# Kernel optimization log

Measured on AMD Instinct MI355X. Metric: run time of the kernel, lower is better.

## Reference

```python
import jax, jax.numpy as jnp
import numpy as np

B, N, M, D = 64, 512, 1024, 128

def setup_inputs() -> dict:
    key = jax.random.key(0)
    ks = jax.random.split(key, 7)
    s = 1.0 / np.sqrt(D)
    return {
        "h_c": jax.random.normal(ks[0], (B, N, D), dtype=jnp.float32),
        "h_p": jax.random.normal(ks[1], (B, M, D), dtype=jnp.float32),
        "U_w": jax.random.normal(ks[2], (D, D), dtype=jnp.float32) * s,
        "U_b": jax.random.normal(ks[3], (D,), dtype=jnp.float32) * s,
        "V_w": jax.random.normal(ks[4], (D, D), dtype=jnp.float32) * s,
        "V_b": jax.random.normal(ks[5], (D,), dtype=jnp.float32) * s,
        "q": jax.random.normal(ks[6], (D,), dtype=jnp.float32),
    }

def reference(h_c, h_p, U_w, U_b, V_w, V_b, q):
    # ReLU-activated linear projections (torch Linear: x @ W.T + b)
    Uc = jax.nn.relu(jnp.einsum('bnd,ed->bne', h_c, U_w) + U_b)  # (B,N,D)
    Vp = jax.nn.relu(jnp.einsum('bmd,ed->bme', h_p, V_w) + V_b)  # (B,M,D)
    # bilinear attention scores and softmax over protein axis
    attn = jnp.einsum('bnd,bmd->bnm', Uc, Vp)                    # (B,N,M)
    weights = jax.nn.softmax(attn, axis=-1)
    context = jnp.einsum('bnm,bmd->bnd', weights, Vp)            # (B,N,D)
    joint = (Uc + context) * q                                   # (B,N,D)
    return joint.mean(axis=1)                                    # (B,D)
```

## Files before the change

kernel.cpp:

```cpp
#include <hip/hip_runtime.h>
#include <hip/hip_bf16.h>
#include <cstdint>

#define BB 64
#define NN 512
#define MM 1024
#define DD 128

typedef __bf16 bf16x8 __attribute__((ext_vector_type(8)));
typedef float f32x4 __attribute__((ext_vector_type(4)));

static __device__ __forceinline__ unsigned short f2bf(float f) {
    union { float f; unsigned int i; } v; v.f = f;
    unsigned int x = v.i;
    x += 0x7FFFu + ((x >> 16) & 1u);
    return (unsigned short)(x >> 16);
}
static __device__ __forceinline__ unsigned int f2bf2(float a, float b) {
    union { __hip_bfloat162 h; unsigned int u; } c;
    c.h = __float22bfloat162_rn(make_float2(a, b));
    return c.u;
}
static __device__ __forceinline__ void async16(const void* g, void* l) {
    __builtin_amdgcn_global_load_lds(
        (const __attribute__((address_space(1))) void*)g,
        (__attribute__((address_space(3))) void*)l, 16, 0, 0);
}

__global__ __launch_bounds__(256, 4) void proj_v_kernel(
    const float* __restrict__ X,
    const float* __restrict__ Wv,
    const float* __restrict__ bias,
    unsigned short* __restrict__ Y,
    unsigned short* __restrict__ YT)
{
    __shared__ __align__(16) unsigned short Ws[128 * 136];
    unsigned short* Ys = Ws;
    unsigned short* Ts = Ws + 8192;
    const int t = threadIdx.x;
    const int lane = t & 63;
    const int wave = t >> 6;
    const int n16 = lane & 15, q = lane >> 4;
    const long row0 = (long)blockIdx.x * 64;

    float4 xv[8];
    {
        const float* xrow = X + (row0 + wave * 16 + n16) * DD + q * 8;
        #pragma unroll
        for (int kk = 0; kk < 4; ++kk) {
            xv[2 * kk]     = *(const float4*)(xrow + kk * 32);
            xv[2 * kk + 1] = *(const float4*)(xrow + kk * 32 + 4);
        }
    }

    {
        const float4* Wg = (const float4*)Wv;
        #pragma unroll
        for (int i = 0; i < 16; ++i) {
            int idx = i * 256 + t;
            float4 v = Wg[idx];
            int off = idx * 4;
            uint2 u = { f2bf2(v.x, v.y), f2bf2(v.z, v.w) };
            *(uint2*)&Ws[(off >> 7) * 136 + (off & 127)] = u;
        }
    }
    __syncthreads();

    f32x4 acc[8];
    #pragma unroll
    for (int j = 0; j < 8; ++j) acc[j] = {0.f, 0.f, 0.f, 0.f};

    #pragma unroll
    for (int kk = 0; kk < 4; ++kk) {
        float4 x0 = xv[2 * kk], x1 = xv[2 * kk + 1];
        union { bf16x8 v; unsigned int u[4]; } a;
        a.u[0] = f2bf2(x0.x, x0.y); a.u[1] = f2bf2(x0.z, x0.w);
        a.u[2] = f2bf2(x1.x, x1.y); a.u[3] = f2bf2(x1.z, x1.w);
        #pragma unroll
        for (int j = 0; j < 8; ++j) {
            bf16x8 b = *(const bf16x8*)&Ws[(j * 16 + n16) * 136 + q * 8 + kk * 32];
            acc[j] = __builtin_amdgcn_mfma_f32_16x16x32_bf16(a.v, b, acc[j], 0, 0, 0);
        }
    }

    unsigned short yb[8][4];
    #pragma unroll
    for (int j = 0; j < 8; ++j) {
        const float bv = bias[j * 16 + n16];
        float y[4];
        #pragma unroll
        for (int r = 0; r < 4; ++r) {
            float v = acc[j][r] + bv;
            y[r] = v > 0.f ? v : 0.f;
        }
        uint2 u = { f2bf2(y[0], y[1]), f2bf2(y[2], y[3]) };
        *(uint2*)&yb[j][0] = u;
    }
    __syncthreads();

    #pragma unroll
    for (int j = 0; j < 8; ++j) {
        const int e = j * 16 + n16;
        #pragma unroll
        for (int r = 0; r < 4; ++r)
            Ys[(wave * 16 + q * 4 + r) * 128 + e] = yb[j][r];
        *(uint2*)&Ts[e * 72 + wave * 16 + q * 4] = *(uint2*)&yb[j][0];
    }
    __syncthreads();

    {
        uint4* dstY = (uint4*)(Y + row0 * DD);
        const long b = row0 >> 10;
        const long mt = (row0 & 1023) >> 6;
        uint4* dstT = (uint4*)(YT + ((b * 16 + mt) * 128) * 64);
        #pragma unroll
        for (int i = 0; i < 4; ++i) {
            int idx = i * 256 + t;
            dstY[idx] = ((const uint4*)Ys)[idx];
            int e = idx >> 3, m = (idx & 7) * 8;
            dstT[idx] = *(const uint4*)&Ts[e * 72 + m];
        }
    }
}

__global__ __launch_bounds__(256, 2) void attn_kernel(
    const float* __restrict__ hc,
    const float* __restrict__ Wu,
    const float* __restrict__ Ub,
    const unsigned short* __restrict__ Vp,
    const unsigned short* __restrict__ VpT,
    float* __restrict__ part)
{
    __shared__ __align__(16) unsigned short smem[37376];
    unsigned short* Ws  = smem;
    unsigned short* Ucs = smem + 17408;
    unsigned short* Ps  = smem + 32768;

    const int t = threadIdx.x;
    const int lane = t & 63;
    const int wave = t >> 6;
    const int n16 = lane & 15, q = lane >> 4;

    const int id = blockIdx.x;
    const int xcd = id & 7;
    const int slot = id >> 3;
    const int b = xcd * 8 + (slot >> 3);
    const int nt = slot & 7;

    const unsigned short* vpb = Vp + (long)b * MM * DD;
    const unsigned short* vtb = VpT + (long)b * MM * DD;

    {
        const float4* Wg = (const float4*)Wu;
        #pragma unroll
        for (int i = 0; i < 16; ++i) {
            int idx = i * 256 + t;
            float4 v = Wg[idx];
            int off = idx * 4;
            uint2 u = { f2bf2(v.x, v.y), f2bf2(v.z, v.w) };
            *(uint2*)&Ws[(off >> 7) * 136 + (off & 127)] = u;
        }
    }
    __syncthreads();

    f32x4 acc[8];
    #pragma unroll
    for (int j = 0; j < 8; ++j) acc[j] = {0.f, 0.f, 0.f, 0.f};
    {
        const float* xrow = hc + ((long)b * NN + nt * 64 + wave * 16 + n16) * DD + q * 8;
        #pragma unroll
        for (int kk = 0; kk < 4; ++kk) {
            float4 x0 = *(const float4*)(xrow + kk * 32);
            float4 x1 = *(const float4*)(xrow + kk * 32 + 4);
            union { bf16x8 v; unsigned int u[4]; } a;
            a.u[0] = f2bf2(x0.x, x0.y); a.u[1] = f2bf2(x0.z, x0.w);
            a.u[2] = f2bf2(x1.x, x1.y); a.u[3] = f2bf2(x1.z, x1.w);
            #pragma unroll
            for (int j = 0; j < 8; ++j) {
                bf16x8 bb = *(const bf16x8*)&Ws[(j * 16 + n16) * 136 + q * 8 + kk * 32];
                acc[j] = __builtin_amdgcn_mfma_f32_16x16x32_bf16(a.v, bb, acc[j], 0, 0, 0);
            }
        }
    }
    float ucred[8];
    #pragma unroll
    for (int j = 0; j < 8; ++j) {
        const float bv = Ub[j * 16 + n16];
        float s = 0.f;
        #pragma unroll
        for (int r = 0; r < 4; ++r) {
            float v = acc[j][r] + bv;
            v = v > 0.f ? v : 0.f;
            s += v;
            Ucs[(wave * 16 + q * 4 + r) * 136 + j * 16 + n16] = f2bf(v);
        }
        ucred[j] = s;
    }
    __syncthreads();

    bf16x8 Bg[4];
    #pragma unroll
    for (int kk = 0; kk < 4; ++kk)
        Bg[kk] = *(const bf16x8*)&Ucs[(wave * 16 + n16) * 136 + q * 8 + kk * 32];

    {
        #pragma unroll
        for (int i = 0; i < 4; ++i) {
            int L = wave * 256 + i * 64 + lane;
            int r = L >> 4, sc = L & 15, c = sc ^ (r & 7);
            async16(vpb + r * 128 + c * 8, smem + wave * 2048 + i * 512);
        }
        #pragma unroll
        for (int i = 0; i < 4; ++i) {
            int L = wave * 256 + i * 64 + lane;
            int r = L >> 3, sc = L & 7, c = sc ^ (r & 7);
            async16(vtb + r * 64 + c * 8, smem + 8192 + wave * 2048 + i * 512);
        }
    }
    __syncthreads();

    f32x4 O[8];
    #pragma unroll
    for (int j = 0; j < 8; ++j) O[j] = {0.f, 0.f, 0.f, 0.f};
    float lpart = 0.f;
    const float LOG2E = 1.44269504088896f;

    for (int mt = 0; mt < 16; ++mt) {
        const unsigned short* Vs  = smem + ((mt & 1) ? 16384 : 0);
        const unsigned short* VTs = Vs + 8192;
        unsigned short* nVs = smem + ((mt & 1) ? 0 : 16384);

        if (mt < 15) {
            const unsigned short* sv = vpb + (mt + 1) * 8192;
            const unsigned short* st = vtb + (mt + 1) * 8192;
            #pragma unroll
            for (int i = 0; i < 4; ++i) {
                int L = wave * 256 + i * 64 + lane;
                int r = L >> 4, sc = L & 15, c = sc ^ (r & 7);
                async16(sv + r * 128 + c * 8, nVs + wave * 2048 + i * 512);
            }
            #pragma unroll
            for (int i = 0; i < 4; ++i) {
                int L = wave * 256 + i * 64 + lane;
                int r = L >> 3, sc = L & 7, c = sc ^ (r & 7);
                async16(st + r * 64 + c * 8, nVs + 8192 + wave * 2048 + i * 512);
            }
        }

        f32x4 S[4];
        #pragma unroll
        for (int j = 0; j < 4; ++j) S[j] = {0.f, 0.f, 0.f, 0.f};
        #pragma unroll
        for (int kk = 0; kk < 4; ++kk) {
            #pragma unroll
            for (int j = 0; j < 4; ++j) {
                int row = j * 16 + n16;
                int col = ((kk * 4 + q) ^ (n16 & 7)) * 8;
                bf16x8 a = *(const bf16x8*)&Vs[row * 128 + col];
                S[j] = __builtin_amdgcn_mfma_f32_16x16x32_bf16(a, Bg[kk], S[j], 0, 0, 0);
            }
        }

        #pragma unroll
        for (int j = 0; j < 4; ++j) {
            float p0 = __builtin_exp2f(S[j][0] * LOG2E);
            float p1 = __builtin_exp2f(S[j][1] * LOG2E);
            float p2 = __builtin_exp2f(S[j][2] * LOG2E);
            float p3 = __builtin_exp2f(S[j][3] * LOG2E);
            lpart += (p0 + p1) + (p2 + p3);
            uint2 u = { f2bf2(p0, p1), f2bf2(p2, p3) };
            *(uint2*)&Ps[wave * 1152 + n16 * 72 + j * 16 + q * 4] = u;
        }

        #pragma unroll
        for (int kk = 0; kk < 2; ++kk) {
            bf16x8 a = *(const bf16x8*)&Ps[wave * 1152 + n16 * 72 + kk * 32 + q * 8];
            #pragma unroll
            for (int j = 0; j < 8; ++j) {
                int row = j * 16 + n16;
                int col = ((kk * 4 + q) ^ (n16 & 7)) * 8;
                bf16x8 bb = *(const bf16x8*)&VTs[row * 64 + col];
                O[j] = __builtin_amdgcn_mfma_f32_16x16x32_bf16(a, bb, O[j], 0, 0, 0);
            }
        }
        __syncthreads();
    }

    lpart += __shfl_xor(lpart, 16);
    lpart += __shfl_xor(lpart, 32);

    float inv[4];
    #pragma unroll
    for (int r = 0; r < 4; ++r)
        inv[r] = 1.0f / __shfl(lpart, q * 4 + r);

    float* red = (float*)Ps;
    #pragma unroll
    for (int j = 0; j < 8; ++j) {
        float s = ucred[j]
                + O[j][0] * inv[0] + O[j][1] * inv[1]
                + O[j][2] * inv[2] + O[j][3] * inv[3];
        s += __shfl_xor(s, 16);
        s += __shfl_xor(s, 32);
        if (q == 0)
            red[wave * 128 + j * 16 + n16] = s;
    }
    __syncthreads();
    if (t < 128) {
        float tot = red[t] + red[128 + t] + red[256 + t] + red[384 + t];
        part[(long)(b * 8 + nt) * DD + t] = tot;
    }
}

__global__ __launch_bounds__(256) void finalize_kernel(
    const float* __restrict__ part, const float* __restrict__ qv,
    float* __restrict__ out)
{
    int i = blockIdx.x * 256 + threadIdx.x;
    int b = i >> 7, d = i & 127;
    const float* p = part + (long)b * 8 * DD + d;
    float s = 0.f;
    #pragma unroll
    for (int nt = 0; nt < 8; ++nt) s += p[nt * DD];
    out[i] = s * qv[d] * (1.0f / (float)NN);
}

extern "C" void kernel_launch(void* const* d_in, const int* in_sizes, int n_in,
                              void* d_out, int out_size, void* d_ws, size_t ws_size,
                              hipStream_t stream) {
    const float* h_c = (const float*)d_in[0];
    const float* h_p = (const float*)d_in[1];
    const float* U_w = (const float*)d_in[2];
    const float* U_b = (const float*)d_in[3];
    const float* V_w = (const float*)d_in[4];
    const float* V_b = (const float*)d_in[5];
    const float* qv  = (const float*)d_in[6];
    float* out = (float*)d_out;

    unsigned short* Vp  = (unsigned short*)d_ws;
    unsigned short* VpT = Vp + (size_t)BB * MM * DD;
    float* part = (float*)(VpT + (size_t)BB * MM * DD);

    proj_v_kernel<<<BB * MM / 64, 256, 0, stream>>>(h_p, V_w, V_b, Vp, VpT);
    attn_kernel<<<512, 256, 0, stream>>>(h_c, U_w, U_b, Vp, VpT, part);
    finalize_kernel<<<32, 256, 0, stream>>>(part, qv, out);
}
```

Before: 130.8 us.

## Split score tile by key rows across waves and fold log2e into Uc

The QK^T-like score stage is repartitioned so each wave loads only its own 16 Vp rows from LDS and multiplies them against all 64 query rows, whose Uc fragments are held in registers (Bg[4][4]). Previously every wave read all 64 Vp rows. The P tile is now shared through LDS across waves, so a block barrier is needed before the PV stage, and the row sums are reduced across waves through LDS at the end. Folding LOG2E into Uc before the bf16 conversion removes a multiply per exp. The costs are more registers, an extra barrier per tile, and a tiny change in rounding.

New measurement: 129.8 us. Within noise of the previous version (-0.8%).

```diff
diff --git a/kernel.cpp b/kernel.cpp
--- a/kernel.cpp
+++ b/kernel.cpp
@@ -150,6 +150,8 @@
     const unsigned short* vpb = Vp + (long)b * MM * DD;
     const unsigned short* vtb = VpT + (long)b * MM * DD;
 
+    const float LOG2E = 1.44269504088896f;
+
     {
         const float4* Wg = (const float4*)Wu;
         #pragma unroll
@@ -192,16 +194,18 @@
             float v = acc[j][r] + bv;
             v = v > 0.f ? v : 0.f;
             s += v;
-            Ucs[(wave * 16 + q * 4 + r) * 136 + j * 16 + n16] = f2bf(v);
+            Ucs[(wave * 16 + q * 4 + r) * 136 + j * 16 + n16] = f2bf(v * LOG2E);
         }
         ucred[j] = s;
     }
     __syncthreads();
 
-    bf16x8 Bg[4];
-    #pragma unroll
-    for (int kk = 0; kk < 4; ++kk)
-        Bg[kk] = *(const bf16x8*)&Ucs[(wave * 16 + n16) * 136 + q * 8 + kk * 32];
+    bf16x8 Bg[4][4];
+    #pragma unroll
+    for (int j = 0; j < 4; ++j)
+        #pragma unroll
+        for (int kk = 0; kk < 4; ++kk)
+            Bg[j][kk] = *(const bf16x8*)&Ucs[(j * 16 + n16) * 136 + q * 8 + kk * 32];
 
     {
         #pragma unroll
@@ -222,13 +226,37 @@
     f32x4 O[8];
     #pragma unroll
     for (int j = 0; j < 8; ++j) O[j] = {0.f, 0.f, 0.f, 0.f};
-    float lpart = 0.f;
-    const float LOG2E = 1.44269504088896f;
+    float lpart[4] = {0.f, 0.f, 0.f, 0.f};
 
     for (int mt = 0; mt < 16; ++mt) {
         const unsigned short* Vs  = smem + ((mt & 1) ? 16384 : 0);
         const unsigned short* VTs = Vs + 8192;
         unsigned short* nVs = smem + ((mt & 1) ? 0 : 16384);
+
+        f32x4 S[4];
+        #pragma unroll
+        for (int j = 0; j < 4; ++j) S[j] = {0.f, 0.f, 0.f, 0.f};
+        #pragma unroll
+        for (int kk = 0; kk < 4; ++kk) {
+            int row = wave * 16 + n16;
+            int col = ((kk * 4 + q) ^ (n16 & 7)) * 8;
+            bf16x8 a = *(const bf16x8*)&Vs[row * 128 + col];
+            #pragma unroll
+            for (int j = 0; j < 4; ++j)
+                S[j] = __builtin_amdgcn_mfma_f32_16x16x32_bf16(a, Bg[j][kk], S[j], 0, 0, 0);
+        }
+
+        #pragma unroll
+        for (int j = 0; j < 4; ++j) {
+            float p0 = __builtin_exp2f(S[j][0]);
+            float p1 = __builtin_exp2f(S[j][1]);
+            float p2 = __builtin_exp2f(S[j][2]);
+            float p3 = __builtin_exp2f(S[j][3]);
+            lpart[j] += (p0 + p1) + (p2 + p3);
+            uint2 u = { f2bf2(p0, p1), f2bf2(p2, p3) };
+            *(uint2*)&Ps[(j * 16 + n16) * 72 + wave * 16 + q * 4] = u;
+        }
+        __syncthreads();
 
         if (mt < 15) {
             const unsigned short* sv = vpb + (mt + 1) * 8192;
@@ -247,34 +275,9 @@
             }
         }
 
-        f32x4 S[4];
-        #pragma unroll
-        for (int j = 0; j < 4; ++j) S[j] = {0.f, 0.f, 0.f, 0.f};
-        #pragma unroll
-        for (int kk = 0; kk < 4; ++kk) {
-            #pragma unroll
-            for (int j = 0; j < 4; ++j) {
-                int row = j * 16 + n16;
-                int col = ((kk * 4 + q) ^ (n16 & 7)) * 8;
-                bf16x8 a = *(const bf16x8*)&Vs[row * 128 + col];
-                S[j] = __builtin_amdgcn_mfma_f32_16x16x32_bf16(a, Bg[kk], S[j], 0, 0, 0);
-            }
-        }
-
-        #pragma unroll
-        for (int j = 0; j < 4; ++j) {
-            float p0 = __builtin_exp2f(S[j][0] * LOG2E);
-            float p1 = __builtin_exp2f(S[j][1] * LOG2E);
-            float p2 = __builtin_exp2f(S[j][2] * LOG2E);
-            float p3 = __builtin_exp2f(S[j][3] * LOG2E);
-            lpart += (p0 + p1) + (p2 + p3);
-            uint2 u = { f2bf2(p0, p1), f2bf2(p2, p3) };
-            *(uint2*)&Ps[wave * 1152 + n16 * 72 + j * 16 + q * 4] = u;
-        }
-
         #pragma unroll
         for (int kk = 0; kk < 2; ++kk) {
-            bf16x8 a = *(const bf16x8*)&Ps[wave * 1152 + n16 * 72 + kk * 32 + q * 8];
+            bf16x8 a = *(const bf16x8*)&Ps[(wave * 16 + n16) * 72 + kk * 32 + q * 8];
             #pragma unroll
             for (int j = 0; j < 8; ++j) {
                 int row = j * 16 + n16;
@@ -286,15 +289,27 @@
         __syncthreads();
     }
 
-    lpart += __shfl_xor(lpart, 16);
-    lpart += __shfl_xor(lpart, 32);
+    #pragma unroll
+    for (int j = 0; j < 4; ++j) {
+        lpart[j] += __shfl_xor(lpart[j], 16);
+        lpart[j] += __shfl_xor(lpart[j], 32);
+    }
+    float* lred = (float*)Ps;
+    float* red  = (float*)Ps + 256;
+    if (q == 0) {
+        #pragma unroll
+        for (int j = 0; j < 4; ++j)
+            lred[wave * 64 + j * 16 + n16] = lpart[j];
+    }
+    __syncthreads();
 
     float inv[4];
     #pragma unroll
-    for (int r = 0; r < 4; ++r)
-        inv[r] = 1.0f / __shfl(lpart, q * 4 + r);
-
-    float* red = (float*)Ps;
+    for (int r = 0; r < 4; ++r) {
+        int n = wave * 16 + q * 4 + r;
+        inv[r] = 1.0f / (lred[n] + lred[64 + n] + lred[128 + n] + lred[192 + n]);
+    }
+
     #pragma unroll
     for (int j = 0; j < 8; ++j) {
         float s = ucred[j]
```

## Read V tiles directly from global memory instead of async LDS staging

Applied to the files above, without the earlier changes.

Removes the double-buffered global_load_lds staging of Vp and VpT tiles and loads MFMA operands straight from global memory, dropping the per-iteration barrier. This shrinks LDS use, so more blocks can be resident per CU, and Ps now reuses the W region. LOG2E is folded into the stored Uc values, which removes the multiply before exp2. The cost is uncoalesced 16-byte global loads that depend on L1/L2 hits, since several blocks read the same batch's Vp.

After: 216.5 us. 1.65x slower.

```diff
diff --git a/kernel.cpp b/kernel.cpp
--- a/kernel.cpp
+++ b/kernel.cpp
@@ -20,11 +20,6 @@
     union { __hip_bfloat162 h; unsigned int u; } c;
     c.h = __float22bfloat162_rn(make_float2(a, b));
     return c.u;
-}
-static __device__ __forceinline__ void async16(const void* g, void* l) {
-    __builtin_amdgcn_global_load_lds(
-        (const __attribute__((address_space(1))) void*)g,
-        (__attribute__((address_space(3))) void*)l, 16, 0, 0);
 }
 
 __global__ __launch_bounds__(256, 4) void proj_v_kernel(
@@ -131,10 +126,10 @@
     const unsigned short* __restrict__ VpT,
     float* __restrict__ part)
 {
-    __shared__ __align__(16) unsigned short smem[37376];
+    __shared__ __align__(16) unsigned short smem[26112];
     unsigned short* Ws  = smem;
     unsigned short* Ucs = smem + 17408;
-    unsigned short* Ps  = smem + 32768;
+    unsigned short* Ps  = smem;
 
     const int t = threadIdx.x;
     const int lane = t & 63;
@@ -149,6 +144,8 @@
 
     const unsigned short* vpb = Vp + (long)b * MM * DD;
     const unsigned short* vtb = VpT + (long)b * MM * DD;
+
+    const float LOG2E = 1.44269504088896f;
 
     {
         const float4* Wg = (const float4*)Wu;
@@ -192,7 +189,7 @@
             float v = acc[j][r] + bv;
             v = v > 0.f ? v : 0.f;
             s += v;
-            Ucs[(wave * 16 + q * 4 + r) * 136 + j * 16 + n16] = f2bf(v);
+            Ucs[(wave * 16 + q * 4 + r) * 136 + j * 16 + n16] = f2bf(v * LOG2E);
         }
         ucred[j] = s;
     }
@@ -203,49 +200,14 @@
     for (int kk = 0; kk < 4; ++kk)
         Bg[kk] = *(const bf16x8*)&Ucs[(wave * 16 + n16) * 136 + q * 8 + kk * 32];
 
-    {
-        #pragma unroll
-        for (int i = 0; i < 4; ++i) {
-            int L = wave * 256 + i * 64 + lane;
-            int r = L >> 4, sc = L & 15, c = sc ^ (r & 7);
-            async16(vpb + r * 128 + c * 8, smem + wave * 2048 + i * 512);
-        }
-        #pragma unroll
-        for (int i = 0; i < 4; ++i) {
-            int L = wave * 256 + i * 64 + lane;
-            int r = L >> 3, sc = L & 7, c = sc ^ (r & 7);
-            async16(vtb + r * 64 + c * 8, smem + 8192 + wave * 2048 + i * 512);
-        }
-    }
-    __syncthreads();
-
     f32x4 O[8];
     #pragma unroll
     for (int j = 0; j < 8; ++j) O[j] = {0.f, 0.f, 0.f, 0.f};
     float lpart = 0.f;
-    const float LOG2E = 1.44269504088896f;
 
     for (int mt = 0; mt < 16; ++mt) {
-        const unsigned short* Vs  = smem + ((mt & 1) ? 16384 : 0);
-        const unsigned short* VTs = Vs + 8192;
-        unsigned short* nVs = smem + ((mt & 1) ? 0 : 16384);
-
-        if (mt < 15) {
-            const unsigned short* sv = vpb + (mt + 1) * 8192;
-            const unsigned short* st = vtb + (mt + 1) * 8192;
-            #pragma unroll
-            for (int i = 0; i < 4; ++i) {
-                int L = wave * 256 + i * 64 + lane;
-                int r = L >> 4, sc = L & 15, c = sc ^ (r & 7);
-                async16(sv + r * 128 + c * 8, nVs + wave * 2048 + i * 512);
-            }
-            #pragma unroll
-            for (int i = 0; i < 4; ++i) {
-                int L = wave * 256 + i * 64 + lane;
-                int r = L >> 3, sc = L & 7, c = sc ^ (r & 7);
-                async16(st + r * 64 + c * 8, nVs + 8192 + wave * 2048 + i * 512);
-            }
-        }
+        const unsigned short* vpt_ = vpb + mt * 8192;
+        const unsigned short* vtt_ = vtb + mt * 8192;
 
         f32x4 S[4];
         #pragma unroll
@@ -254,19 +216,17 @@
         for (int kk = 0; kk < 4; ++kk) {
             #pragma unroll
             for (int j = 0; j < 4; ++j) {
-                int row = j * 16 + n16;
-                int col = ((kk * 4 + q) ^ (n16 & 7)) * 8;
-                bf16x8 a = *(const bf16x8*)&Vs[row * 128 + col];
+                bf16x8 a = *(const bf16x8*)&vpt_[(j * 16 + n16) * 128 + kk * 32 + q * 8];
                 S[j] = __builtin_amdgcn_mfma_f32_16x16x32_bf16(a, Bg[kk], S[j], 0, 0, 0);
             }
         }
 
         #pragma unroll
         for (int j = 0; j < 4; ++j) {
-            float p0 = __builtin_exp2f(S[j][0] * LOG2E);
-            float p1 = __builtin_exp2f(S[j][1] * LOG2E);
-            float p2 = __builtin_exp2f(S[j][2] * LOG2E);
-            float p3 = __builtin_exp2f(S[j][3] * LOG2E);
+            float p0 = __builtin_exp2f(S[j][0]);
+            float p1 = __builtin_exp2f(S[j][1]);
+            float p2 = __builtin_exp2f(S[j][2]);
+            float p3 = __builtin_exp2f(S[j][3]);
             lpart += (p0 + p1) + (p2 + p3);
             uint2 u = { f2bf2(p0, p1), f2bf2(p2, p3) };
             *(uint2*)&Ps[wave * 1152 + n16 * 72 + j * 16 + q * 4] = u;
@@ -277,13 +237,10 @@
             bf16x8 a = *(const bf16x8*)&Ps[wave * 1152 + n16 * 72 + kk * 32 + q * 8];
             #pragma unroll
             for (int j = 0; j < 8; ++j) {
-                int row = j * 16 + n16;
-                int col = ((kk * 4 + q) ^ (n16 & 7)) * 8;
-                bf16x8 bb = *(const bf16x8*)&VTs[row * 64 + col];
+                bf16x8 bb = *(const bf16x8*)&vtt_[(j * 16 + n16) * 64 + kk * 32 + q * 8];
                 O[j] = __builtin_amdgcn_mfma_f32_16x16x32_bf16(a, bb, O[j], 0, 0, 0);
             }
         }
-        __syncthreads();
     }
 
     lpart += __shfl_xor(lpart, 16);
@@ -294,7 +251,7 @@
     for (int r = 0; r < 4; ++r)
         inv[r] = 1.0f / __shfl(lpart, q * 4 + r);
 
-    float* red = (float*)Ps;
+    float* red = (float*)(smem + 4608);
     #pragma unroll
     for (int j = 0; j < 8; ++j) {
         float s = ucred[j]
```
